# Performance work log

Measured on AMD Instinct MI355X. Metric: run time of the kernel, lower is better.

Reference implementation:

```python
import jax, jax.numpy as jnp
import numpy as np

N_NODES = 100000
F_IN, HID, OUT = 128, 64, 32


def setup_inputs() -> dict:
    key = jax.random.key(0)
    ks = jax.random.split(key, 16)
    x = jax.random.normal(ks[0], (N_NODES, F_IN), dtype=jnp.float32)
    edge_index = jax.random.randint(ks[1], (2, 3200000), 0, N_NODES, dtype=jnp.int64)
    edge_label_index = jax.random.randint(ks[2], (2, 1000000), 0, N_NODES, dtype=jnp.int64)
    def glorot(k, shape):
        lim = float(np.sqrt(6.0 / (shape[0] + shape[1])))
        return jax.random.uniform(k, shape, jnp.float32, -lim, lim)
    W1 = glorot(ks[3], (F_IN, HID)); b1 = jnp.zeros((HID,), jnp.float32)
    W2 = glorot(ks[4], (HID, HID)); b2 = jnp.zeros((HID,), jnp.float32)
    W3 = glorot(ks[5], (HID, OUT)); b3 = jnp.zeros((OUT,), jnp.float32)
    lpW1 = glorot(ks[6], (2 * OUT, HID)); lpb1 = jnp.zeros((HID,), jnp.float32)
    lpW2 = glorot(ks[7], (HID, 1)); lpb2 = jnp.zeros((1,), jnp.float32)
    return dict(x=x, edge_index=edge_index, edge_label_index=edge_label_index,
                W1=W1, b1=b1, W2=W2, b2=b2, W3=W3, b3=b3,
                lpW1=lpW1, lpb1=lpb1, lpW2=lpW2, lpb2=lpb2)


def _gcn_norm(edge_index, num_nodes):
    # PyG GCNConv default: add self-loops, symmetric normalization.
    self_loops = jnp.arange(num_nodes, dtype=edge_index.dtype)
    row = jnp.concatenate([edge_index[0], self_loops])  # source nodes
    col = jnp.concatenate([edge_index[1], self_loops])  # target nodes
    deg = jax.ops.segment_sum(jnp.ones_like(col, dtype=jnp.float32), col,
                              num_segments=num_nodes)
    dinv = jnp.where(deg > 0, jax.lax.rsqrt(deg), 0.0)
    norm = dinv[row] * dinv[col]  # [E + N]
    return row, col, norm


def _gcn_layer(x, W, b, row, col, norm, num_nodes):
    h = x @ W                               # [N, out]
    msg = h[row] * norm[:, None]            # gather + scale per edge
    agg = jax.ops.segment_sum(msg, col, num_segments=num_nodes)
    return agg + b


def reference(x, edge_index, edge_label_index, W1, b1, W2, b2, W3, b3,
              lpW1, lpb1, lpW2, lpb2):
    n = x.shape[0]
    row, col, norm = _gcn_norm(edge_index, n)
    # encode (eval mode: dropout is identity)
    z = jax.nn.relu(_gcn_layer(x, W1, b1, row, col, norm, n))
    z = jax.nn.relu(_gcn_layer(z, W2, b2, row, col, norm, n))
    z = _gcn_layer(z, W3, b3, row, col, norm, n)
    # decode: gather endpoint embeddings + MLP link predictor
    ef = jnp.concatenate([z[edge_label_index[0]], z[edge_label_index[1]]], axis=1)
    h = jax.nn.relu(ef @ lpW1 + lpb1)
    link_pred = h @ lpW2 + lpb2             # [E_label, 1]
    return link_pred, z
```

## Files before the change

### kernel.cpp

```cpp
#include <hip/hip_runtime.h>
#include <hip/hip_bf16.h>
#include <hip/hip_fp16.h>


#define BINA_CHUNK 8192


__global__ __launch_bounds__(512) void bhist_kernel(const int* __restrict__ colv,
                                                    int* __restrict__ chist,
                                                    int E, int nbuk) {
    __shared__ int hist[800];
    int base = blockIdx.x * BINA_CHUNK;
    int end = min(base + BINA_CHUNK, E);
    for (int i = threadIdx.x; i < nbuk; i += 512) hist[i] = 0;
    __syncthreads();
    int e = base + threadIdx.x * 4;
    for (; e + 4 <= end; e += 2048) {
        int4 c4 = *(const int4*)&colv[e];
        atomicAdd(&hist[c4.x >> 7], 1);
        atomicAdd(&hist[c4.y >> 7], 1);
        atomicAdd(&hist[c4.z >> 7], 1);
        atomicAdd(&hist[c4.w >> 7], 1);
    }
    for (; e < end; ++e) atomicAdd(&hist[colv[e] >> 7], 1);
    __syncthreads();
    for (int b = threadIdx.x; b < nbuk; b += 512)
        chist[(size_t)blockIdx.x * nbuk + b] = hist[b];
}


__global__ __launch_bounds__(256) void colscan_kernel(int* __restrict__ chist,
                                                      int* __restrict__ bcount,
                                                      int nchunk, int nbuk) {
    __shared__ int sh[256];
    const int b = blockIdx.x;
    const int c0 = threadIdx.x * 4;
    int v[4]; int s = 0;
#pragma unroll
    for (int i = 0; i < 4; ++i) {
        int c = c0 + i;
        v[i] = (c < nchunk) ? chist[(size_t)c * nbuk + b] : 0;
        s += v[i];
    }
    sh[threadIdx.x] = s;
    __syncthreads();
#pragma unroll
    for (int off = 1; off < 256; off <<= 1) {
        int y = (threadIdx.x >= (unsigned)off) ? sh[threadIdx.x - off] : 0;
        __syncthreads();
        sh[threadIdx.x] += y;
        __syncthreads();
    }
    int ex = sh[threadIdx.x] - s;
#pragma unroll
    for (int i = 0; i < 4; ++i) {
        int c = c0 + i;
        if (c < nchunk) { chist[(size_t)c * nbuk + b] = ex; ex += v[i]; }
    }
    if (threadIdx.x == 255) bcount[b] = sh[255];
}


__global__ __launch_bounds__(256) void bscan_kernel(const int* __restrict__ bcount,
                                                    int* __restrict__ bbase,
                                                    int nbuk, int* __restrict__ offsets, int N) {
    __shared__ int sh[256];
    int base = threadIdx.x * 4;
    int v[4]; int tsum = 0;
#pragma unroll
    for (int i = 0; i < 4; ++i) { int idx = base + i; v[i] = (idx < nbuk) ? bcount[idx] : 0; tsum += v[i]; }
    sh[threadIdx.x] = tsum;
    __syncthreads();
#pragma unroll
    for (int off = 1; off < 256; off <<= 1) {
        int y = (threadIdx.x >= (unsigned)off) ? sh[threadIdx.x - off] : 0;
        __syncthreads();
        sh[threadIdx.x] += y;
        __syncthreads();
    }
    int ex = sh[threadIdx.x] - tsum;
#pragma unroll
    for (int i = 0; i < 4; ++i) {
        int idx = base + i;
        if (idx < nbuk) { bbase[idx] = ex; ex += v[i]; }
        else if (idx == nbuk) { bbase[idx] = ex; offsets[N] = ex; }
    }
}


__global__ __launch_bounds__(512) void binA_kernel(const int* __restrict__ rowv,
                                                   const int* __restrict__ colv,
                                                   const int* __restrict__ chist,
                                                   const int* __restrict__ bbase,
                                                   int* __restrict__ pairs,
                                                   int E, int nbuk) {
    __shared__ int pos[800];
    int base = blockIdx.x * BINA_CHUNK;
    int end = min(base + BINA_CHUNK, E);
    for (int b = threadIdx.x; b < nbuk; b += 512)
        pos[b] = bbase[b] + chist[(size_t)blockIdx.x * nbuk + b];
    __syncthreads();
    int e = base + threadIdx.x * 4;
    for (; e + 4 <= end; e += 2048) {
        int4 c4 = *(const int4*)&colv[e];
        int4 r4 = *(const int4*)&rowv[e];
        int g0 = atomicAdd(&pos[c4.x >> 7], 1); pairs[g0] = (r4.x << 7) | (c4.x & 127);
        int g1 = atomicAdd(&pos[c4.y >> 7], 1); pairs[g1] = (r4.y << 7) | (c4.y & 127);
        int g2 = atomicAdd(&pos[c4.z >> 7], 1); pairs[g2] = (r4.z << 7) | (c4.z & 127);
        int g3 = atomicAdd(&pos[c4.w >> 7], 1); pairs[g3] = (r4.w << 7) | (c4.w & 127);
    }
    for (; e < end; ++e) {
        int c = colv[e];
        int g = atomicAdd(&pos[c >> 7], 1);
        pairs[g] = (rowv[e] << 7) | (c & 127);
    }
}


__global__ __launch_bounds__(512) void binB_kernel(const int* __restrict__ pairs,
                                                   const int* __restrict__ bbase,
                                                   int* __restrict__ offsets,
                                                   float* __restrict__ dinv,
                                                   int* __restrict__ edge_src, int N) {
    __shared__ int lcnt[128];
    __shared__ int sc[128];
    __shared__ int lcur[128];
    int nodeBeg = blockIdx.x << 7;
    int segBeg = bbase[blockIdx.x];
    int segEnd = bbase[blockIdx.x + 1];
    if (threadIdx.x < 128) lcnt[threadIdx.x] = 0;
    __syncthreads();
    for (int e = segBeg + threadIdx.x; e < segEnd; e += 512)
        atomicAdd(&lcnt[pairs[e] & 127], 1);
    __syncthreads();
    int v = (threadIdx.x < 128) ? lcnt[threadIdx.x] : 0;
    if (threadIdx.x < 128) sc[threadIdx.x] = v;
    __syncthreads();
    for (int off = 1; off < 128; off <<= 1) {
        int y = 0;
        if (threadIdx.x < 128 && threadIdx.x >= (unsigned)off) y = sc[threadIdx.x - off];
        __syncthreads();
        if (threadIdx.x < 128) sc[threadIdx.x] += y;
        __syncthreads();
    }
    if (threadIdx.x < 128) {
        int ex = sc[threadIdx.x] - v;
        lcur[threadIdx.x] = ex;
        int node = nodeBeg + threadIdx.x;
        if (node < N) {
            offsets[node] = segBeg + ex;
            dinv[node] = rsqrtf((float)(v + 1));
        }
    }
    __syncthreads();
    for (int e = segBeg + threadIdx.x; e < segEnd; e += 512) {
        int p = pairs[e];
        int rel = atomicAdd(&lcur[p & 127], 1);
        edge_src[segBeg + rel] = p >> 7;
    }
}


template <int K, int NOUT>
__global__ __launch_bounds__(32 * (NOUT / 4)) void gemm_scale(const float* __restrict__ in_,
                                                              const float* __restrict__ W,
                                                              const float* __restrict__ dinv,
                                                              __half* __restrict__ out, int N) {
    constexpr int TPB = 32 * (NOUT / 4);
    constexpr int KS = (K > 64) ? 64 : K;
    constexpr int XPITCH = KS + 4;
    __shared__ float xs[64 * XPITCH];
    __shared__ float ws[KS * NOUT];

    const int tid = threadIdx.x;
    const int nodeBase = blockIdx.x * 64;

    const int jg = tid % (NOUT / 4);
    const int ng = tid / (NOUT / 4);

    float acc[2][4];
#pragma unroll
    for (int i = 0; i < 2; ++i)
#pragma unroll
        for (int j = 0; j < 4; ++j) acc[i][j] = 0.f;

    for (int kh = 0; kh < K / KS; ++kh) {
        if (kh) __syncthreads();
        for (int i = tid; i < KS * NOUT / 4; i += TPB)
            *(float4*)&ws[i * 4] = *(const float4*)&W[(size_t)kh * KS * NOUT + i * 4];
        for (int i = tid; i < 64 * KS / 4; i += TPB) {
            int row = i / (KS / 4), c = i % (KS / 4);
            int src = nodeBase + row; if (src >= N) src = N - 1;
            *(float4*)&xs[row * XPITCH + c * 4] =
                *(const float4*)&in_[(size_t)src * K + kh * KS + c * 4];
        }
        __syncthreads();

#pragma unroll 4
        for (int kc = 0; kc < KS / 4; ++kc) {
            float4 xv[2], wv[4];
#pragma unroll
            for (int ni = 0; ni < 2; ++ni)
                xv[ni] = *(const float4*)&xs[(ng * 2 + ni) * XPITCH + kc * 4];
#pragma unroll
            for (int t = 0; t < 4; ++t)
                wv[t] = *(const float4*)&ws[(kc * 4 + t) * NOUT + jg * 4];
#pragma unroll
            for (int ni = 0; ni < 2; ++ni) {
                acc[ni][0] = fmaf(xv[ni].x, wv[0].x, acc[ni][0]);
                acc[ni][1] = fmaf(xv[ni].x, wv[0].y, acc[ni][1]);
                acc[ni][2] = fmaf(xv[ni].x, wv[0].z, acc[ni][2]);
                acc[ni][3] = fmaf(xv[ni].x, wv[0].w, acc[ni][3]);
                acc[ni][0] = fmaf(xv[ni].y, wv[1].x, acc[ni][0]);
                acc[ni][1] = fmaf(xv[ni].y, wv[1].y, acc[ni][1]);
                acc[ni][2] = fmaf(xv[ni].y, wv[1].z, acc[ni][2]);
                acc[ni][3] = fmaf(xv[ni].y, wv[1].w, acc[ni][3]);
                acc[ni][0] = fmaf(xv[ni].z, wv[2].x, acc[ni][0]);
                acc[ni][1] = fmaf(xv[ni].z, wv[2].y, acc[ni][1]);
                acc[ni][2] = fmaf(xv[ni].z, wv[2].z, acc[ni][2]);
                acc[ni][3] = fmaf(xv[ni].z, wv[2].w, acc[ni][3]);
                acc[ni][0] = fmaf(xv[ni].w, wv[3].x, acc[ni][0]);
                acc[ni][1] = fmaf(xv[ni].w, wv[3].y, acc[ni][1]);
                acc[ni][2] = fmaf(xv[ni].w, wv[3].z, acc[ni][2]);
                acc[ni][3] = fmaf(xv[ni].w, wv[3].w, acc[ni][3]);
            }
        }
    }

#pragma unroll
    for (int ni = 0; ni < 2; ++ni) {
        int node = nodeBase + ng * 2 + ni;
        if (node < N) {
            float dn = dinv[node];
            __half2* op = (__half2*)(out + (size_t)node * NOUT + jg * 4);
            op[0] = __floats2half2_rn(acc[ni][0] * dn, acc[ni][1] * dn);
            op[1] = __floats2half2_rn(acc[ni][2] * dn, acc[ni][3] * dn);
        }
    }
}


template <int F, bool RELU>
__global__ __launch_bounds__(256) void agg_pull(const __half* __restrict__ h,
                                                const float* __restrict__ dinv,
                                                const float* __restrict__ bias,
                                                const int* __restrict__ edge_src,
                                                const int* __restrict__ offsets,
                                                float* __restrict__ out, int N) {
    constexpr int LPN = F / 8;
    constexpr int GPW = 64 / LPN;
    constexpr int UNR = LPN;
    int lane = threadIdx.x & 63;
    int wave = (blockIdx.x * 256 + (int)threadIdx.x) >> 6;
    int g = lane / LPN;
    int fl = lane % LPN;
    int gbase = lane & ~(LPN - 1);
    int node = wave * GPW + g;
    if (node >= N) return;
    float dn = dinv[node];
    int beg = offsets[node], end = offsets[node + 1];
    const float4* __restrict__ hp4 = (const float4*)h;

    float4 sv = hp4[(size_t)node * LPN + fl];
    float2 s0 = __half22float2(*(const __half2*)&sv.x);
    float2 s1 = __half22float2(*(const __half2*)&sv.y);
    float2 s2 = __half22float2(*(const __half2*)&sv.z);
    float2 s3 = __half22float2(*(const __half2*)&sv.w);
    float aA[8] = {s0.x, s0.y, s1.x, s1.y, s2.x, s2.y, s3.x, s3.y};
    float aB[8] = {0.f, 0.f, 0.f, 0.f, 0.f, 0.f, 0.f, 0.f};

    int j = beg;
    for (; j + UNR <= end; j += UNR) {
        int smy = edge_src[j + fl];
        int sk[UNR];
#pragma unroll
        for (int k = 0; k < UNR; ++k)
            sk[k] = __shfl(smy, gbase + k, 64);
        float4 v[UNR];
#pragma unroll
        for (int k = 0; k < UNR; ++k)
            v[k] = hp4[(size_t)sk[k] * LPN + fl];
#pragma unroll
        for (int k = 0; k < UNR; ++k) {
            float2 p0 = __half22float2(*(const __half2*)&v[k].x);
            float2 p1 = __half22float2(*(const __half2*)&v[k].y);
            float2 p2 = __half22float2(*(const __half2*)&v[k].z);
            float2 p3 = __half22float2(*(const __half2*)&v[k].w);
            float* a = (k & 1) ? aB : aA;
            a[0] += p0.x; a[1] += p0.y; a[2] += p1.x; a[3] += p1.y;
            a[4] += p2.x; a[5] += p2.y; a[6] += p3.x; a[7] += p3.y;
        }
    }
    if (j < end) {
        int r = end - j;
        int smy = (fl < r) ? edge_src[j + fl] : 0;
        for (int k = 0; k < r; ++k) {
            int sk = __shfl(smy, gbase + k, 64);
            float4 v = hp4[(size_t)sk * LPN + fl];
            float2 p0 = __half22float2(*(const __half2*)&v.x);
            float2 p1 = __half22float2(*(const __half2*)&v.y);
            float2 p2 = __half22float2(*(const __half2*)&v.z);
            float2 p3 = __half22float2(*(const __half2*)&v.w);
            float* a = (k & 1) ? aB : aA;
            a[0] += p0.x; a[1] += p0.y; a[2] += p1.x; a[3] += p1.y;
            a[4] += p2.x; a[5] += p2.y; a[6] += p3.x; a[7] += p3.y;
        }
    }

    float4 bva = *(const float4*)&bias[fl * 8];
    float4 bvb = *(const float4*)&bias[fl * 8 + 4];
    float r0 = (aA[0] + aB[0]) * dn + bva.x;
    float r1 = (aA[1] + aB[1]) * dn + bva.y;
    float r2 = (aA[2] + aB[2]) * dn + bva.z;
    float r3 = (aA[3] + aB[3]) * dn + bva.w;
    float r4 = (aA[4] + aB[4]) * dn + bvb.x;
    float r5 = (aA[5] + aB[5]) * dn + bvb.y;
    float r6 = (aA[6] + aB[6]) * dn + bvb.z;
    float r7 = (aA[7] + aB[7]) * dn + bvb.w;
    if (RELU) {
        r0 = fmaxf(r0, 0.f); r1 = fmaxf(r1, 0.f); r2 = fmaxf(r2, 0.f); r3 = fmaxf(r3, 0.f);
        r4 = fmaxf(r4, 0.f); r5 = fmaxf(r5, 0.f); r6 = fmaxf(r6, 0.f); r7 = fmaxf(r7, 0.f);
    }
    float* op = &out[(size_t)node * F + fl * 8];
    *(float4*)op = make_float4(r0, r1, r2, r3);
    *(float4*)(op + 4) = make_float4(r4, r5, r6, r7);
}


__global__ __launch_bounds__(512) void gemm_uv(const float* __restrict__ z,
                                               const float* __restrict__ W1,
                                               __half* __restrict__ uv, int N) {
    constexpr int ZPITCH = 36;
    __shared__ float zs[64 * ZPITCH];
    __shared__ float ws[64 * 64];
    const int tid = threadIdx.x;
    const int nodeBase = blockIdx.x * 64;

    for (int i = tid; i < 64 * 64 / 4; i += 512)
        *(float4*)&ws[i * 4] = *(const float4*)&W1[i * 4];
    for (int i = tid; i < 64 * 8; i += 512) {
        int row = i / 8, c = i % 8;
        int src = nodeBase + row; if (src >= N) src = N - 1;
        *(float4*)&zs[row * ZPITCH + c * 4] = *(const float4*)&z[(size_t)src * 32 + c * 4];
    }
    __syncthreads();

    const int jg = tid % 16;
    const int ng = tid / 16;

    float au[2][4], av[2][4];
#pragma unroll
    for (int i = 0; i < 2; ++i)
#pragma unroll
        for (int j = 0; j < 4; ++j) { au[i][j] = 0.f; av[i][j] = 0.f; }

#pragma unroll 4
    for (int kc = 0; kc < 8; ++kc) {
        float4 xv[2], wu[4], wv2[4];
#pragma unroll
        for (int ni = 0; ni < 2; ++ni)
            xv[ni] = *(const float4*)&zs[(ng * 2 + ni) * ZPITCH + kc * 4];
#pragma unroll
        for (int t = 0; t < 4; ++t) {
            wu[t]  = *(const float4*)&ws[(kc * 4 + t) * 64 + jg * 4];
            wv2[t] = *(const float4*)&ws[(32 + kc * 4 + t) * 64 + jg * 4];
        }
#pragma unroll
        for (int ni = 0; ni < 2; ++ni) {
            float xk[4] = {xv[ni].x, xv[ni].y, xv[ni].z, xv[ni].w};
#pragma unroll
            for (int t = 0; t < 4; ++t) {
                au[ni][0] = fmaf(xk[t], wu[t].x, au[ni][0]);
                au[ni][1] = fmaf(xk[t], wu[t].y, au[ni][1]);
                au[ni][2] = fmaf(xk[t], wu[t].z, au[ni][2]);
                au[ni][3] = fmaf(xk[t], wu[t].w, au[ni][3]);
                av[ni][0] = fmaf(xk[t], wv2[t].x, av[ni][0]);
                av[ni][1] = fmaf(xk[t], wv2[t].y, av[ni][1]);
                av[ni][2] = fmaf(xk[t], wv2[t].z, av[ni][2]);
                av[ni][3] = fmaf(xk[t], wv2[t].w, av[ni][3]);
            }
        }
    }

#pragma unroll
    for (int ni = 0; ni < 2; ++ni) {
        int node = nodeBase + ng * 2 + ni;
        if (node < N) {
            __half2* pu = (__half2*)(uv + (size_t)node * 128 + jg * 4);
            pu[0] = __floats2half2_rn(au[ni][0], au[ni][1]);
            pu[1] = __floats2half2_rn(au[ni][2], au[ni][3]);
            __half2* pv = (__half2*)(uv + (size_t)node * 128 + 64 + jg * 4);
            pv[0] = __floats2half2_rn(av[ni][0], av[ni][1]);
            pv[1] = __floats2half2_rn(av[ni][2], av[ni][3]);
        }
    }
}


__global__ __launch_bounds__(256) void decode_edge(const __half* __restrict__ uv,
                                                   const int* __restrict__ eli, int EL,
                                                   const float* __restrict__ lpb1,
                                                   const float* __restrict__ lpW2,
                                                   const float* __restrict__ lpb2,
                                                   float* __restrict__ out) {
    const int sub = threadIdx.x & 7;
    float4 b1a = *(const float4*)&lpb1[sub * 8];
    float4 b1b = *(const float4*)&lpb1[sub * 8 + 4];
    float4 w2a = *(const float4*)&lpW2[sub * 8];
    float4 w2b = *(const float4*)&lpW2[sub * 8 + 4];
    const float b2v = lpb2[0];
    int e = blockIdx.x * 32 + (threadIdx.x >> 3);
    if (e >= EL) return;
    int a = eli[e], b = eli[EL + e];
    float4 ra = *(const float4*)(uv + (size_t)a * 128 + sub * 8);
    float4 rb = *(const float4*)(uv + (size_t)b * 128 + 64 + sub * 8);
    float2 a01 = __half22float2(*(const __half2*)&ra.x);
    float2 a23 = __half22float2(*(const __half2*)&ra.y);
    float2 a45 = __half22float2(*(const __half2*)&ra.z);
    float2 a67 = __half22float2(*(const __half2*)&ra.w);
    float2 b01 = __half22float2(*(const __half2*)&rb.x);
    float2 b23 = __half22float2(*(const __half2*)&rb.y);
    float2 b45 = __half22float2(*(const __half2*)&rb.z);
    float2 b67 = __half22float2(*(const __half2*)&rb.w);
    float p = fmaxf(a01.x + b01.x + b1a.x, 0.f) * w2a.x;
    p = fmaf(fmaxf(a01.y + b01.y + b1a.y, 0.f), w2a.y, p);
    p = fmaf(fmaxf(a23.x + b23.x + b1a.z, 0.f), w2a.z, p);
    p = fmaf(fmaxf(a23.y + b23.y + b1a.w, 0.f), w2a.w, p);
    p = fmaf(fmaxf(a45.x + b45.x + b1b.x, 0.f), w2b.x, p);
    p = fmaf(fmaxf(a45.y + b45.y + b1b.y, 0.f), w2b.y, p);
    p = fmaf(fmaxf(a67.x + b67.x + b1b.z, 0.f), w2b.z, p);
    p = fmaf(fmaxf(a67.y + b67.y + b1b.w, 0.f), w2b.w, p);
    p += __shfl_down(p, 4, 8);
    p += __shfl_down(p, 2, 8);
    p += __shfl_down(p, 1, 8);
    if (sub == 0) out[e] = p + b2v;
}


extern "C" void kernel_launch(void* const* d_in, const int* in_sizes, int n_in,
                              void* d_out, int out_size, void* d_ws, size_t ws_size,
                              hipStream_t stream) {
    const float* x    = (const float*)d_in[0];
    const int* ei     = (const int*)d_in[1];
    const int* eli    = (const int*)d_in[2];
    const float* W1   = (const float*)d_in[3];
    const float* b1   = (const float*)d_in[4];
    const float* W2   = (const float*)d_in[5];
    const float* b2   = (const float*)d_in[6];
    const float* W3   = (const float*)d_in[7];
    const float* b3   = (const float*)d_in[8];
    const float* lpW1 = (const float*)d_in[9];
    const float* lpb1 = (const float*)d_in[10];
    const float* lpW2 = (const float*)d_in[11];
    const float* lpb2 = (const float*)d_in[12];

    const int N  = in_sizes[0] / 128;
    const int E  = in_sizes[1] / 2;
    const int EL = in_sizes[2] / 2;

    char* p = (char*)d_ws;
    auto alloc = [&](size_t bytes) { void* r = (void*)p; p += (bytes + 255) & ~(size_t)255; return r; };
    float* dinv     = (float*)alloc((size_t)N * 4);
    int*   offsets  = (int*)alloc((size_t)(N + 1) * 4);
    int*   bcount   = (int*)alloc(1024 * 4);
    int*   bbase    = (int*)alloc(1024 * 4);
    int*   edge_src = (int*)alloc((size_t)E * 4);
    __half* bufG    = (__half*)alloc((size_t)N * 64 * 2);
    float* bufZ     = (float*)alloc((size_t)N * 64 * 4);
    __half* uvbuf   = (__half*)alloc((size_t)N * 128 * 2);
    int*   pairs    = (int*)uvbuf;
    int*   chist    = (int*)bufZ;

    const int* rowv = ei;
    const int* colv = ei + E;

    int nbuk = (N + 127) / 128;
    int nchunk = (E + BINA_CHUNK - 1) / BINA_CHUNK;

    bhist_kernel<<<nchunk, 512, 0, stream>>>(colv, chist, E, nbuk);
    colscan_kernel<<<nbuk, 256, 0, stream>>>(chist, bcount, nchunk, nbuk);
    bscan_kernel<<<1, 256, 0, stream>>>(bcount, bbase, nbuk, offsets, N);
    binA_kernel<<<nchunk, 512, 0, stream>>>(rowv, colv, chist, bbase, pairs, E, nbuk);
    binB_kernel<<<nbuk, 512, 0, stream>>>(pairs, bbase, offsets, dinv, edge_src, N);

    float* zout = (float*)d_out + EL;

    int gblocks = (N + 63) / 64;

    int aggblocks64 = (N + 31) / 32;
    int aggblocks32 = (N + 63) / 64;

    gemm_scale<128, 64><<<gblocks, 512, 0, stream>>>(x, W1, dinv, bufG, N);
    agg_pull<64, true><<<aggblocks64, 256, 0, stream>>>(bufG, dinv, b1, edge_src, offsets, bufZ, N);
    gemm_scale<64, 64><<<gblocks, 512, 0, stream>>>(bufZ, W2, dinv, bufG, N);
    agg_pull<64, true><<<aggblocks64, 256, 0, stream>>>(bufG, dinv, b2, edge_src, offsets, bufZ, N);
    gemm_scale<64, 32><<<gblocks, 256, 0, stream>>>(bufZ, W3, dinv, bufG, N);
    agg_pull<32, false><<<aggblocks32, 256, 0, stream>>>(bufG, dinv, b3, edge_src, offsets, zout, N);
    gemm_uv<<<gblocks, 512, 0, stream>>>(zout, lpW1, uvbuf, N);
    decode_edge<<<(EL + 31) / 32, 256, 0, stream>>>(uvbuf, eli, EL, lpb1, lpW2, lpb2, (float*)d_out);
}
```

Before: 457.8 us.

## Use packed float2 math in GEMMs/aggregation and cache bin pairs in LDS

Replaces scalar fmaf accumulations in gemm_scale, gemm_uv and the agg_pull accumulators with two-wide float vector types, so the compiler can emit packed FP32 instructions (v_pk_fma/v_pk_add) on CDNA. Separately, binB_kernel now stages each bucket's pairs in a 24KB shared buffer during the counting pass and reuses them in the scatter pass, avoiding a second global read when the segment fits. The extra LDS may lower occupancy of binB, and packing relies on the compiler's codegen choices.

```diff
diff --git a/kernel.cpp b/kernel.cpp
--- a/kernel.cpp
+++ b/kernel.cpp
@@ -4,6 +4,8 @@
 
 
 #define BINA_CHUNK 8192
+
+typedef float v2f __attribute__((ext_vector_type(2)));
 
 
 __global__ __launch_bounds__(512) void bhist_kernel(const int* __restrict__ colv,
@@ -125,13 +127,19 @@
     __shared__ int lcnt[128];
     __shared__ int sc[128];
     __shared__ int lcur[128];
+    __shared__ int sp[6144];
     int nodeBeg = blockIdx.x << 7;
     int segBeg = bbase[blockIdx.x];
     int segEnd = bbase[blockIdx.x + 1];
+    int len = segEnd - segBeg;
+    bool fit = (len <= 6144);
     if (threadIdx.x < 128) lcnt[threadIdx.x] = 0;
     __syncthreads();
-    for (int e = segBeg + threadIdx.x; e < segEnd; e += 512)
-        atomicAdd(&lcnt[pairs[e] & 127], 1);
+    for (int i = threadIdx.x; i < len; i += 512) {
+        int p = pairs[segBeg + i];
+        if (fit) sp[i] = p;
+        atomicAdd(&lcnt[p & 127], 1);
+    }
     __syncthreads();
     int v = (threadIdx.x < 128) ? lcnt[threadIdx.x] : 0;
     if (threadIdx.x < 128) sc[threadIdx.x] = v;
@@ -153,8 +161,8 @@
         }
     }
     __syncthreads();
-    for (int e = segBeg + threadIdx.x; e < segEnd; e += 512) {
-        int p = pairs[e];
+    for (int i = threadIdx.x; i < len; i += 512) {
+        int p = fit ? sp[i] : pairs[segBeg + i];
         int rel = atomicAdd(&lcur[p & 127], 1);
         edge_src[segBeg + rel] = p >> 7;
     }
@@ -178,11 +186,11 @@
     const int jg = tid % (NOUT / 4);
     const int ng = tid / (NOUT / 4);
 
-    float acc[2][4];
+    v2f acc[2][2];
 #pragma unroll
     for (int i = 0; i < 2; ++i)
 #pragma unroll
-        for (int j = 0; j < 4; ++j) acc[i][j] = 0.f;
+        for (int j = 0; j < 2; ++j) acc[i][j] = (v2f){0.f, 0.f};
 
     for (int kh = 0; kh < K / KS; ++kh) {
         if (kh) __syncthreads();
@@ -207,22 +215,15 @@
                 wv[t] = *(const float4*)&ws[(kc * 4 + t) * NOUT + jg * 4];
 #pragma unroll
             for (int ni = 0; ni < 2; ++ni) {
-                acc[ni][0] = fmaf(xv[ni].x, wv[0].x, acc[ni][0]);
-                acc[ni][1] = fmaf(xv[ni].x, wv[0].y, acc[ni][1]);
-                acc[ni][2] = fmaf(xv[ni].x, wv[0].z, acc[ni][2]);
-                acc[ni][3] = fmaf(xv[ni].x, wv[0].w, acc[ni][3]);
-                acc[ni][0] = fmaf(xv[ni].y, wv[1].x, acc[ni][0]);
-                acc[ni][1] = fmaf(xv[ni].y, wv[1].y, acc[ni][1]);
-                acc[ni][2] = fmaf(xv[ni].y, wv[1].z, acc[ni][2]);
-                acc[ni][3] = fmaf(xv[ni].y, wv[1].w, acc[ni][3]);
-                acc[ni][0] = fmaf(xv[ni].z, wv[2].x, acc[ni][0]);
-                acc[ni][1] = fmaf(xv[ni].z, wv[2].y, acc[ni][1]);
-                acc[ni][2] = fmaf(xv[ni].z, wv[2].z, acc[ni][2]);
-                acc[ni][3] = fmaf(xv[ni].z, wv[2].w, acc[ni][3]);
-                acc[ni][0] = fmaf(xv[ni].w, wv[3].x, acc[ni][0]);
-                acc[ni][1] = fmaf(xv[ni].w, wv[3].y, acc[ni][1]);
-                acc[ni][2] = fmaf(xv[ni].w, wv[3].z, acc[ni][2]);
-                acc[ni][3] = fmaf(xv[ni].w, wv[3].w, acc[ni][3]);
+                float xk[4] = {xv[ni].x, xv[ni].y, xv[ni].z, xv[ni].w};
+#pragma unroll
+                for (int t = 0; t < 4; ++t) {
+                    v2f xb = {xk[t], xk[t]};
+                    v2f wlo = {wv[t].x, wv[t].y};
+                    v2f whi = {wv[t].z, wv[t].w};
+                    acc[ni][0] += xb * wlo;
+                    acc[ni][1] += xb * whi;
+                }
             }
         }
     }
@@ -233,8 +234,8 @@
         if (node < N) {
             float dn = dinv[node];
             __half2* op = (__half2*)(out + (size_t)node * NOUT + jg * 4);
-            op[0] = __floats2half2_rn(acc[ni][0] * dn, acc[ni][1] * dn);
-            op[1] = __floats2half2_rn(acc[ni][2] * dn, acc[ni][3] * dn);
+            op[0] = __floats2half2_rn(acc[ni][0].x * dn, acc[ni][0].y * dn);
+            op[1] = __floats2half2_rn(acc[ni][1].x * dn, acc[ni][1].y * dn);
         }
     }
 }
@@ -266,8 +267,8 @@
     float2 s1 = __half22float2(*(const __half2*)&sv.y);
     float2 s2 = __half22float2(*(const __half2*)&sv.z);
     float2 s3 = __half22float2(*(const __half2*)&sv.w);
-    float aA[8] = {s0.x, s0.y, s1.x, s1.y, s2.x, s2.y, s3.x, s3.y};
-    float aB[8] = {0.f, 0.f, 0.f, 0.f, 0.f, 0.f, 0.f, 0.f};
+    v2f aA[4] = {{s0.x, s0.y}, {s1.x, s1.y}, {s2.x, s2.y}, {s3.x, s3.y}};
+    v2f aB[4] = {{0.f, 0.f}, {0.f, 0.f}, {0.f, 0.f}, {0.f, 0.f}};
 
     int j = beg;
     for (; j + UNR <= end; j += UNR) {
@@ -286,9 +287,11 @@
             float2 p1 = __half22float2(*(const __half2*)&v[k].y);
             float2 p2 = __half22float2(*(const __half2*)&v[k].z);
             float2 p3 = __half22float2(*(const __half2*)&v[k].w);
-            float* a = (k & 1) ? aB : aA;
-            a[0] += p0.x; a[1] += p0.y; a[2] += p1.x; a[3] += p1.y;
-            a[4] += p2.x; a[5] += p2.y; a[6] += p3.x; a[7] += p3.y;
+            v2f* a = (k & 1) ? aB : aA;
+            a[0] += (v2f){p0.x, p0.y};
+            a[1] += (v2f){p1.x, p1.y};
+            a[2] += (v2f){p2.x, p2.y};
+            a[3] += (v2f){p3.x, p3.y};
         }
     }
     if (j < end) {
@@ -301,22 +304,28 @@
             float2 p1 = __half22float2(*(const __half2*)&v.y);
             float2 p2 = __half22float2(*(const __half2*)&v.z);
             float2 p3 = __half22float2(*(const __half2*)&v.w);
-            float* a = (k & 1) ? aB : aA;
-            a[0] += p0.x; a[1] += p0.y; a[2] += p1.x; a[3] += p1.y;
-            a[4] += p2.x; a[5] += p2.y; a[6] += p3.x; a[7] += p3.y;
+            v2f* a = (k & 1) ? aB : aA;
+            a[0] += (v2f){p0.x, p0.y};
+            a[1] += (v2f){p1.x, p1.y};
+            a[2] += (v2f){p2.x, p2.y};
+            a[3] += (v2f){p3.x, p3.y};
         }
     }
 
     float4 bva = *(const float4*)&bias[fl * 8];
     float4 bvb = *(const float4*)&bias[fl * 8 + 4];
-    float r0 = (aA[0] + aB[0]) * dn + bva.x;
-    float r1 = (aA[1] + aB[1]) * dn + bva.y;
-    float r2 = (aA[2] + aB[2]) * dn + bva.z;
-    float r3 = (aA[3] + aB[3]) * dn + bva.w;
-    float r4 = (aA[4] + aB[4]) * dn + bvb.x;
-    float r5 = (aA[5] + aB[5]) * dn + bvb.y;
-    float r6 = (aA[6] + aB[6]) * dn + bvb.z;
-    float r7 = (aA[7] + aB[7]) * dn + bvb.w;
+    v2f t0 = aA[0] + aB[0];
+    v2f t1 = aA[1] + aB[1];
+    v2f t2 = aA[2] + aB[2];
+    v2f t3 = aA[3] + aB[3];
+    float r0 = t0.x * dn + bva.x;
+    float r1 = t0.y * dn + bva.y;
+    float r2 = t1.x * dn + bva.z;
+    float r3 = t1.y * dn + bva.w;
+    float r4 = t2.x * dn + bvb.x;
+    float r5 = t2.y * dn + bvb.y;
+    float r6 = t3.x * dn + bvb.z;
+    float r7 = t3.y * dn + bvb.w;
     if (RELU) {
         r0 = fmaxf(r0, 0.f); r1 = fmaxf(r1, 0.f); r2 = fmaxf(r2, 0.f); r3 = fmaxf(r3, 0.f);
         r4 = fmaxf(r4, 0.f); r5 = fmaxf(r5, 0.f); r6 = fmaxf(r6, 0.f); r7 = fmaxf(r7, 0.f);
@@ -348,11 +357,11 @@
     const int jg = tid % 16;
     const int ng = tid / 16;
 
-    float au[2][4], av[2][4];
+    v2f au[2][2], av[2][2];
 #pragma unroll
     for (int i = 0; i < 2; ++i)
 #pragma unroll
-        for (int j = 0; j < 4; ++j) { au[i][j] = 0.f; av[i][j] = 0.f; }
+        for (int j = 0; j < 2; ++j) { au[i][j] = (v2f){0.f, 0.f}; av[i][j] = (v2f){0.f, 0.f}; }
 
 #pragma unroll 4
     for (int kc = 0; kc < 8; ++kc) {
@@ -370,14 +379,11 @@
             float xk[4] = {xv[ni].x, xv[ni].y, xv[ni].z, xv[ni].w};
 #pragma unroll
             for (int t = 0; t < 4; ++t) {
-                au[ni][0] = fmaf(xk[t], wu[t].x, au[ni][0]);
-                au[ni][1] = fmaf(xk[t], wu[t].y, au[ni][1]);
-                au[ni][2] = fmaf(xk[t], wu[t].z, au[ni][2]);
-                au[ni][3] = fmaf(xk[t], wu[t].w, au[ni][3]);
-                av[ni][0] = fmaf(xk[t], wv2[t].x, av[ni][0]);
-                av[ni][1] = fmaf(xk[t], wv2[t].y, av[ni][1]);
-                av[ni][2] = fmaf(xk[t], wv2[t].z, av[ni][2]);
-                av[ni][3] = fmaf(xk[t], wv2[t].w, av[ni][3]);
+                v2f xb = {xk[t], xk[t]};
+                au[ni][0] += xb * (v2f){wu[t].x, wu[t].y};
+                au[ni][1] += xb * (v2f){wu[t].z, wu[t].w};
+                av[ni][0] += xb * (v2f){wv2[t].x, wv2[t].y};
+                av[ni][1] += xb * (v2f){wv2[t].z, wv2[t].w};
             }
         }
     }
@@ -387,11 +393,11 @@
         int node = nodeBase + ng * 2 + ni;
         if (node < N) {
             __half2* pu = (__half2*)(uv + (size_t)node * 128 + jg * 4);
-            pu[0] = __floats2half2_rn(au[ni][0], au[ni][1]);
-            pu[1] = __floats2half2_rn(au[ni][2], au[ni][3]);
+            pu[0] = __floats2half2_rn(au[ni][0].x, au[ni][0].y);
+            pu[1] = __floats2half2_rn(au[ni][1].x, au[ni][1].y);
             __half2* pv = (__half2*)(uv + (size_t)node * 128 + 64 + jg * 4);
-            pv[0] = __floats2half2_rn(av[ni][0], av[ni][1]);
-            pv[1] = __floats2half2_rn(av[ni][2], av[ni][3]);
+            pv[0] = __floats2half2_rn(av[ni][0].x, av[ni][0].y);
+            pv[1] = __floats2half2_rn(av[ni][1].x, av[ni][1].y);
         }
     }
 }
```

Result: no change. 466.6 us (+1.9%).
